# Kernel optimization log

Hardware: AMD Instinct MI355X
Metric: run time of the kernel (lower is better)

Reference implementation:

```python
import jax, jax.numpy as jnp
import numpy as np

TEMPERATURE = 0.5
EPS = 1e-8  # torch CosineSimilarity eps


def setup_inputs() -> dict:
    key = jax.random.key(0)
    k1, k2 = jax.random.split(key)
    N, D = 4096, 256
    z1 = jax.random.normal(k1, (N, D), dtype=jnp.float32)
    z2 = jax.random.normal(k2, (N, D), dtype=jnp.float32)
    return {"z1": z1, "z2": z2}


def reference(z1, z2):
    N = z1.shape[0]
    z = jnp.concatenate([z1, z2], axis=0)  # [2N, D]
    # cosine similarity = normalized dot products (GEMM instead of O(N^2 D) broadcast)
    norm = jnp.linalg.norm(z, axis=-1, keepdims=True)
    zn = z / jnp.maximum(norm, EPS)
    sim = (zn @ zn.T) / TEMPERATURE  # [2N, 2N]
    # mask self-similarity on the diagonal
    idx = jnp.arange(2 * N)
    sim = jnp.where(idx[:, None] == idx[None, :], -jnp.inf, sim)
    # target[i] = (i - N) mod 2N  (arange(2N).roll(N))
    target = jnp.roll(idx, N)
    logp = jax.nn.log_softmax(sim, axis=-1)
    loss = -jnp.mean(logp[idx, target])
    return loss
```

## Files before the change

kernel.cpp:

```cpp
#include <hip/hip_runtime.h>

typedef __bf16 bf16x8 __attribute__((ext_vector_type(8)));
typedef float f32x4 __attribute__((ext_vector_type(4)));

#define TWO_LOG2E 2.88539008177792681f

#define GLOADLDS16(g, l) __builtin_amdgcn_global_load_lds(                     \
    (const __attribute__((address_space(1))) void*)(g),                        \
    (__attribute__((address_space(3))) void*)(l), 16, 0, 0)

__device__ __forceinline__ unsigned f2bf(float f) {
    unsigned u = __float_as_uint(f);
    return (u + 0x7FFFu + ((u >> 16) & 1u)) >> 16;
}

__global__ void __launch_bounds__(256) normalize_kernel(
    const float* __restrict__ z1, const float* __restrict__ z2,
    unsigned short* __restrict__ zn, float* __restrict__ S, float* __restrict__ out)
{
    if (blockIdx.x < 32) S[(blockIdx.x << 8) + threadIdx.x] = 0.f;
    if (blockIdx.x == 32 && threadIdx.x == 0) out[0] = 0.f;

    const int wave = threadIdx.x >> 6, lane = threadIdx.x & 63;
    const int row = (blockIdx.x << 2) + wave;
    const float* src = (row < 4096) ? (z1 + row * 256) : (z2 + (row - 4096) * 256);
    float4 v = ((const float4*)src)[lane];
    float ss = v.x * v.x + v.y * v.y + v.z * v.z + v.w * v.w;
#pragma unroll
    for (int m = 32; m > 0; m >>= 1) ss += __shfl_xor(ss, m, 64);
    float sc = 1.0f / fmaxf(sqrtf(ss), 1e-8f);
    uint2 w;
    w.x = f2bf(v.x * sc) | (f2bf(v.y * sc) << 16);
    w.y = f2bf(v.z * sc) | (f2bf(v.w * sc) << 16);
    *(uint2*)(zn + row * 256 + (lane << 2)) = w;
}

__global__ void __launch_bounds__(64, 2) simexp_kernel(
    const unsigned short* __restrict__ zn, float* __restrict__ S)
{
    __shared__ __align__(16) unsigned short Bs[4][1024];

    const int lane = threadIdx.x;
    const int q = lane >> 4, n16 = lane & 15;
    const int job = blockIdx.x;
    const int rowBase = (job >> 4) << 6;
    const int colRun  = (job & 15) << 9;

    bf16x8 a[4][8];
#pragma unroll
    for (int rt = 0; rt < 4; ++rt)
#pragma unroll
        for (int ks = 0; ks < 8; ++ks)
            a[rt][ks] = *(const bf16x8*)(zn + ((rowBase + (rt << 4) + n16) << 8)
                                            + (ks << 5) + (q << 3));

    auto stage = [&](int m) {
        const int colBase = colRun + ((m >> 3) << 5);
        const int koff = (m & 7) << 5;
        unsigned short* base = (unsigned short*)&Bs[0][0] + ((m & 3) << 10);
#pragma unroll
        for (int p = 0; p < 2; ++p) {
            int s = (p << 6) + lane;
            int c = s >> 2, d = s & 3;
            int k8 = d ^ (c & 3);
            GLOADLDS16(zn + ((colBase + c) << 8) + koff + (k8 << 3), base + (s << 3));
        }
    };

    float rs[4][4];
#pragma unroll
    for (int i = 0; i < 4; ++i)
#pragma unroll
        for (int j = 0; j < 4; ++j) rs[i][j] = 0.f;

    f32x4 acc[4][2];
    auto consume = [&](int m) {
        const unsigned short* bb = (const unsigned short*)&Bs[0][0] + ((m & 3) << 10);
        const int kc = m & 7;
        bf16x8 bf[2];
#pragma unroll
        for (int ct = 0; ct < 2; ++ct) {
            int c = (ct << 4) + n16;
            int d = q ^ (c & 3);
            bf[ct] = *(const bf16x8*)(bb + (((c << 2) | d) << 3));
        }
#pragma unroll
        for (int rt = 0; rt < 4; ++rt)
#pragma unroll
            for (int ct = 0; ct < 2; ++ct)
                acc[rt][ct] = __builtin_amdgcn_mfma_f32_16x16x32_bf16(
                    a[rt][kc], bf[ct], acc[rt][ct], 0, 0, 0);
    };
    auto acczero = [&]() {
#pragma unroll
        for (int rt = 0; rt < 4; ++rt)
#pragma unroll
            for (int ct = 0; ct < 2; ++ct) acc[rt][ct] = (f32x4){0.f, 0.f, 0.f, 0.f};
    };
    auto epilogue = [&]() {
#pragma unroll
        for (int rt = 0; rt < 4; ++rt)
#pragma unroll
            for (int ct = 0; ct < 2; ++ct)
#pragma unroll
                for (int r = 0; r < 4; ++r)
                    rs[rt][r] += __builtin_amdgcn_exp2f(acc[rt][ct][r] * TWO_LOG2E);
    };

    stage(0); stage(1); stage(2);

    for (int cc = 0; cc < 15; ++cc) {
        acczero();
#pragma unroll
        for (int kc = 0; kc < 8; ++kc) {
            int m = (cc << 3) + kc;
            stage(m + 3);
            asm volatile("s_waitcnt vmcnt(6)" ::: "memory");
            consume(m);
        }
        epilogue();
    }
    acczero();
#pragma unroll
    for (int kc = 0; kc < 5; ++kc) {
        int m = 120 + kc;
        stage(m + 3);
        asm volatile("s_waitcnt vmcnt(6)" ::: "memory");
        consume(m);
    }
    asm volatile("s_waitcnt vmcnt(4)" ::: "memory");
    consume(125);
    asm volatile("s_waitcnt vmcnt(2)" ::: "memory");
    consume(126);
    asm volatile("s_waitcnt vmcnt(0)" ::: "memory");
    consume(127);
    epilogue();

#pragma unroll
    for (int rt = 0; rt < 4; ++rt)
#pragma unroll
        for (int r = 0; r < 4; ++r) {
            float s = rs[rt][r];
            s += __shfl_xor(s, 1, 64);
            s += __shfl_xor(s, 2, 64);
            s += __shfl_xor(s, 4, 64);
            s += __shfl_xor(s, 8, 64);
            if (n16 == 0) atomicAdd(&S[rowBase + (rt << 4) + (q << 2) + r], s);
        }
}

__global__ void __launch_bounds__(256) finish_kernel(
    const unsigned short* __restrict__ zn, const float* __restrict__ S,
    float* __restrict__ out)
{
    __shared__ float vals[16];
    const int tid = threadIdx.x, lane = tid & 63, wave = tid >> 6;
    const int q = lane >> 4, n16 = lane & 15;
    const int rib = (wave << 2) + q;
    const int row = (blockIdx.x << 4) + rib;
    const int tar = (row + 4096) & 8191;

    float drr = 0.f, drt = 0.f;
#pragma unroll
    for (int i = 0; i < 4; ++i) {
        int k = (i << 6) + (n16 << 2);
        uint2 ur = *(const uint2*)(zn + (row << 8) + k);
        uint2 ut = *(const uint2*)(zn + (tar << 8) + k);
        float a0 = __uint_as_float(ur.x << 16),  a1 = __uint_as_float(ur.x & 0xFFFF0000u);
        float a2 = __uint_as_float(ur.y << 16),  a3 = __uint_as_float(ur.y & 0xFFFF0000u);
        float b0 = __uint_as_float(ut.x << 16),  b1 = __uint_as_float(ut.x & 0xFFFF0000u);
        float b2 = __uint_as_float(ut.y << 16),  b3 = __uint_as_float(ut.y & 0xFFFF0000u);
        drr += a0 * a0 + a1 * a1 + a2 * a2 + a3 * a3;
        drt += a0 * b0 + a1 * b1 + a2 * b2 + a3 * b3;
    }
#pragma unroll
    for (int m = 1; m <= 8; m <<= 1) {
        drr += __shfl_xor(drr, m, 64);
        drt += __shfl_xor(drt, m, 64);
    }
    if (n16 == 0) {
        float Sv = S[row] - __builtin_amdgcn_exp2f(drr * TWO_LOG2E);
        vals[rib] = 0.693147180559945f * __builtin_amdgcn_logf(Sv) - 2.0f * drt;
    }
    __syncthreads();
    if (tid == 0) {
        float s = 0.f;
#pragma unroll
        for (int i = 0; i < 16; ++i) s += vals[i];
        atomicAdd(out, s * (1.0f / 8192.0f));
    }
}

extern "C" void kernel_launch(void* const* d_in, const int* in_sizes, int n_in,
                              void* d_out, int out_size, void* d_ws, size_t ws_size,
                              hipStream_t stream)
{
    const float* z1 = (const float*)d_in[0];
    const float* z2 = (const float*)d_in[1];
    unsigned short* zn = (unsigned short*)d_ws;
    float* S = (float*)((char*)d_ws + 8192 * 256 * sizeof(unsigned short));
    float* out = (float*)d_out;

    normalize_kernel<<<2048, 256, 0, stream>>>(z1, z2, zn, S, out);
    simexp_kernel<<<2048, 64, 0, stream>>>(zn, S);
    finish_kernel<<<512, 256, 0, stream>>>(zn, S, out);
}
```

Measured before the change: 106.8 us.

## Fuse normalize, sim-exp and finish into one cooperative kernel with grid syncs

Merges the three kernels into a single cooperative launch of 512 blocks of 256 threads, with each wave running one former simexp job and grid-wide syncs between the normalize, GEMM-exp and finish phases. This removes two kernel launch boundaries and their gaps. In exchange, parallelism drops from 2048 single-wave blocks to 512 four-wave blocks that must all be co-resident, and grid syncs add barrier cost. Host-side device queries also add per-call overhead, and the old three-kernel path stays as a fallback.

Measured after the change: 105.8 us. About the same (-0.9%).

```diff
diff --git a/kernel.cpp b/kernel.cpp
--- a/kernel.cpp
+++ b/kernel.cpp
@@ -1,4 +1,7 @@
 #include <hip/hip_runtime.h>
+#include <hip/hip_cooperative_groups.h>
+
+namespace cg = cooperative_groups;
 
 typedef __bf16 bf16x8 __attribute__((ext_vector_type(8)));
 typedef float f32x4 __attribute__((ext_vector_type(4)));
@@ -14,35 +17,12 @@
     return (u + 0x7FFFu + ((u >> 16) & 1u)) >> 16;
 }
 
-__global__ void __launch_bounds__(256) normalize_kernel(
-    const float* __restrict__ z1, const float* __restrict__ z2,
-    unsigned short* __restrict__ zn, float* __restrict__ S, float* __restrict__ out)
-{
-    if (blockIdx.x < 32) S[(blockIdx.x << 8) + threadIdx.x] = 0.f;
-    if (blockIdx.x == 32 && threadIdx.x == 0) out[0] = 0.f;
-
-    const int wave = threadIdx.x >> 6, lane = threadIdx.x & 63;
-    const int row = (blockIdx.x << 2) + wave;
-    const float* src = (row < 4096) ? (z1 + row * 256) : (z2 + (row - 4096) * 256);
-    float4 v = ((const float4*)src)[lane];
-    float ss = v.x * v.x + v.y * v.y + v.z * v.z + v.w * v.w;
-#pragma unroll
-    for (int m = 32; m > 0; m >>= 1) ss += __shfl_xor(ss, m, 64);
-    float sc = 1.0f / fmaxf(sqrtf(ss), 1e-8f);
-    uint2 w;
-    w.x = f2bf(v.x * sc) | (f2bf(v.y * sc) << 16);
-    w.y = f2bf(v.z * sc) | (f2bf(v.w * sc) << 16);
-    *(uint2*)(zn + row * 256 + (lane << 2)) = w;
-}
-
-__global__ void __launch_bounds__(64, 2) simexp_kernel(
-    const unsigned short* __restrict__ zn, float* __restrict__ S)
-{
-    __shared__ __align__(16) unsigned short Bs[4][1024];
-
-    const int lane = threadIdx.x;
+__device__ __forceinline__ void simexp_wave(const unsigned short* __restrict__ zn,
+                                            float* __restrict__ S,
+                                            unsigned short* __restrict__ ring,
+                                            int job, int lane)
+{
     const int q = lane >> 4, n16 = lane & 15;
-    const int job = blockIdx.x;
     const int rowBase = (job >> 4) << 6;
     const int colRun  = (job & 15) << 9;
 
@@ -57,7 +37,7 @@
     auto stage = [&](int m) {
         const int colBase = colRun + ((m >> 3) << 5);
         const int koff = (m & 7) << 5;
-        unsigned short* base = (unsigned short*)&Bs[0][0] + ((m & 3) << 10);
+        unsigned short* base = ring + ((m & 3) << 10);
 #pragma unroll
         for (int p = 0; p < 2; ++p) {
             int s = (p << 6) + lane;
@@ -75,7 +55,7 @@
 
     f32x4 acc[4][2];
     auto consume = [&](int m) {
-        const unsigned short* bb = (const unsigned short*)&Bs[0][0] + ((m & 3) << 10);
+        const unsigned short* bb = ring + ((m & 3) << 10);
         const int kc = m & 7;
         bf16x8 bf[2];
 #pragma unroll
@@ -149,17 +129,43 @@
         }
 }
 
-__global__ void __launch_bounds__(256) finish_kernel(
-    const unsigned short* __restrict__ zn, const float* __restrict__ S,
-    float* __restrict__ out)
-{
-    __shared__ float vals[16];
+__global__ void __launch_bounds__(256, 2) ntxent_fused(
+    const float* __restrict__ z1, const float* __restrict__ z2,
+    unsigned short* __restrict__ zn, float* __restrict__ S, float* __restrict__ out)
+{
+    __shared__ __align__(16) unsigned short Bs[4][4][1024];
+
     const int tid = threadIdx.x, lane = tid & 63, wave = tid >> 6;
     const int q = lane >> 4, n16 = lane & 15;
+    const int b = blockIdx.x;
+
+    if (tid < 16) S[(b << 4) + tid] = 0.f;
+    if (b == 0 && tid == 0) out[0] = 0.f;
+#pragma unroll
+    for (int r = 0; r < 4; ++r) {
+        int row = (b << 4) + (wave << 2) + r;
+        const float* src = (row < 4096) ? (z1 + row * 256) : (z2 + (row - 4096) * 256);
+        float4 v = ((const float4*)src)[lane];
+        float ss = v.x * v.x + v.y * v.y + v.z * v.z + v.w * v.w;
+#pragma unroll
+        for (int m = 32; m > 0; m >>= 1) ss += __shfl_xor(ss, m, 64);
+        float sc = 1.0f / fmaxf(sqrtf(ss), 1e-8f);
+        uint2 w;
+        w.x = f2bf(v.x * sc) | (f2bf(v.y * sc) << 16);
+        w.y = f2bf(v.z * sc) | (f2bf(v.w * sc) << 16);
+        *(uint2*)(zn + row * 256 + (lane << 2)) = w;
+    }
+
+    cg::this_grid().sync();
+
+    simexp_wave(zn, S, &Bs[wave][0][0], (b << 2) | wave, lane);
+
+    cg::this_grid().sync();
+
+    float* vals = (float*)&Bs[0][0][0];
     const int rib = (wave << 2) + q;
-    const int row = (blockIdx.x << 4) + rib;
+    const int row = (b << 4) + rib;
     const int tar = (row + 4096) & 8191;
-
     float drr = 0.f, drt = 0.f;
 #pragma unroll
     for (int i = 0; i < 4; ++i) {
@@ -178,6 +184,75 @@
         drr += __shfl_xor(drr, m, 64);
         drt += __shfl_xor(drt, m, 64);
     }
+    __syncthreads();
+    if (n16 == 0) {
+        float Sv = S[row] - __builtin_amdgcn_exp2f(drr * TWO_LOG2E);
+        vals[rib] = 0.693147180559945f * __builtin_amdgcn_logf(Sv) - 2.0f * drt;
+    }
+    __syncthreads();
+    if (tid == 0) {
+        float s = 0.f;
+#pragma unroll
+        for (int i = 0; i < 16; ++i) s += vals[i];
+        atomicAdd(out, s * (1.0f / 8192.0f));
+    }
+}
+
+__global__ void __launch_bounds__(256) normalize_kernel(
+    const float* __restrict__ z1, const float* __restrict__ z2,
+    unsigned short* __restrict__ zn, float* __restrict__ S, float* __restrict__ out)
+{
+    if (blockIdx.x < 32) S[(blockIdx.x << 8) + threadIdx.x] = 0.f;
+    if (blockIdx.x == 32 && threadIdx.x == 0) out[0] = 0.f;
+    const int wave = threadIdx.x >> 6, lane = threadIdx.x & 63;
+    const int row = (blockIdx.x << 2) + wave;
+    const float* src = (row < 4096) ? (z1 + row * 256) : (z2 + (row - 4096) * 256);
+    float4 v = ((const float4*)src)[lane];
+    float ss = v.x * v.x + v.y * v.y + v.z * v.z + v.w * v.w;
+#pragma unroll
+    for (int m = 32; m > 0; m >>= 1) ss += __shfl_xor(ss, m, 64);
+    float sc = 1.0f / fmaxf(sqrtf(ss), 1e-8f);
+    uint2 w;
+    w.x = f2bf(v.x * sc) | (f2bf(v.y * sc) << 16);
+    w.y = f2bf(v.z * sc) | (f2bf(v.w * sc) << 16);
+    *(uint2*)(zn + row * 256 + (lane << 2)) = w;
+}
+
+__global__ void __launch_bounds__(64, 2) simexp_kernel(
+    const unsigned short* __restrict__ zn, float* __restrict__ S)
+{
+    __shared__ __align__(16) unsigned short Bs[4][1024];
+    simexp_wave(zn, S, &Bs[0][0], blockIdx.x, threadIdx.x);
+}
+
+__global__ void __launch_bounds__(256) finish_kernel(
+    const unsigned short* __restrict__ zn, const float* __restrict__ S,
+    float* __restrict__ out)
+{
+    __shared__ float vals[16];
+    const int tid = threadIdx.x, lane = tid & 63, wave = tid >> 6;
+    const int q = lane >> 4, n16 = lane & 15;
+    const int rib = (wave << 2) + q;
+    const int row = (blockIdx.x << 4) + rib;
+    const int tar = (row + 4096) & 8191;
+    float drr = 0.f, drt = 0.f;
+#pragma unroll
+    for (int i = 0; i < 4; ++i) {
+        int k = (i << 6) + (n16 << 2);
+        uint2 ur = *(const uint2*)(zn + (row << 8) + k);
+        uint2 ut = *(const uint2*)(zn + (tar << 8) + k);
+        float a0 = __uint_as_float(ur.x << 16),  a1 = __uint_as_float(ur.x & 0xFFFF0000u);
+        float a2 = __uint_as_float(ur.y << 16),  a3 = __uint_as_float(ur.y & 0xFFFF0000u);
+        float b0 = __uint_as_float(ut.x << 16),  b1 = __uint_as_float(ut.x & 0xFFFF0000u);
+        float b2 = __uint_as_float(ut.y << 16),  b3 = __uint_as_float(ut.y & 0xFFFF0000u);
+        drr += a0 * a0 + a1 * a1 + a2 * a2 + a3 * a3;
+        drt += a0 * b0 + a1 * b1 + a2 * b2 + a3 * b3;
+    }
+#pragma unroll
+    for (int m = 1; m <= 8; m <<= 1) {
+        drr += __shfl_xor(drr, m, 64);
+        drt += __shfl_xor(drt, m, 64);
+    }
     if (n16 == 0) {
         float Sv = S[row] - __builtin_amdgcn_exp2f(drr * TWO_LOG2E);
         vals[rib] = 0.693147180559945f * __builtin_amdgcn_logf(Sv) - 2.0f * drt;
@@ -201,6 +276,21 @@
     float* S = (float*)((char*)d_ws + 8192 * 256 * sizeof(unsigned short));
     float* out = (float*)d_out;
 
+    int dev = 0;
+    hipGetDevice(&dev);
+    int coopOK = 0;
+    hipDeviceGetAttribute(&coopOK, hipDeviceAttributeCooperativeLaunch, dev);
+    int cus = 0;
+    hipDeviceGetAttribute(&cus, hipDeviceAttributeMultiprocessorCount, dev);
+    int maxB = 0;
+    hipOccupancyMaxActiveBlocksPerMultiprocessor(&maxB, ntxent_fused, 256, 0);
+
+    if (coopOK && (long long)maxB * cus >= 512) {
+        void* args[] = {(void*)&z1, (void*)&z2, (void*)&zn, (void*)&S, (void*)&out};
+        hipError_t err = hipLaunchCooperativeKernel(ntxent_fused, dim3(512), dim3(256),
+                                                    args, 0, stream);
+        if (err == hipSuccess) return;
+    }
     normalize_kernel<<<2048, 256, 0, stream>>>(z1, z2, zn, S, out);
     simexp_kernel<<<2048, 64, 0, stream>>>(zn, S);
     finish_kernel<<<512, 256, 0, stream>>>(zn, S, out);
```

## Exploit symmetry of similarity matrix to compute only upper-triangular tiles

Applied to the files above, without the earlier changes.

The exp-sum kernel now computes only the upper-triangular blocks of the symmetric similarity matrix. Each tile's exponentials are added both to its row sums and, via column sums reduced across lanes, to the sums of the transposed rows. Diagonal-straddling tiles mask entries by index so nothing is counted twice. This roughly halves the MFMA and exp work in exchange for extra column-sum atomics, a per-element index compare on diagonal tiles, and a 2112-block grid of half-length column runs.

After: 144.6 us. +35.3%, slower.

```diff
diff --git a/kernel.cpp b/kernel.cpp
--- a/kernel.cpp
+++ b/kernel.cpp
@@ -42,9 +42,14 @@
 
     const int lane = threadIdx.x;
     const int q = lane >> 4, n16 = lane & 15;
-    const int job = blockIdx.x;
-    const int rowBase = (job >> 4) << 6;
-    const int colRun  = (job & 15) << 9;
+
+    int t = blockIdx.x, v = 0;
+    while (t >= ((32 - v) << 2)) { t -= (32 - v) << 2; ++v; }
+    const int si = (v << 2) + t / (32 - v);
+    const int rn = v + t % (32 - v);
+    const int rowBase = si << 6;
+    const int colRun  = rn << 8;
+    const bool strad = (rn == v);
 
     bf16x8 a[4][8];
 #pragma unroll
@@ -68,10 +73,13 @@
     };
 
     float rs[4][4];
+    float cs[16];
 #pragma unroll
     for (int i = 0; i < 4; ++i)
 #pragma unroll
         for (int j = 0; j < 4; ++j) rs[i][j] = 0.f;
+#pragma unroll
+    for (int i = 0; i < 16; ++i) cs[i] = 0.f;
 
     f32x4 acc[4][2];
     auto consume = [&](int m) {
@@ -97,19 +105,38 @@
 #pragma unroll
             for (int ct = 0; ct < 2; ++ct) acc[rt][ct] = (f32x4){0.f, 0.f, 0.f, 0.f};
     };
-    auto epilogue = [&]() {
-#pragma unroll
-        for (int rt = 0; rt < 4; ++rt)
-#pragma unroll
-            for (int ct = 0; ct < 2; ++ct)
-#pragma unroll
-                for (int r = 0; r < 4; ++r)
-                    rs[rt][r] += __builtin_amdgcn_exp2f(acc[rt][ct][r] * TWO_LOG2E);
+    auto epilogue = [&](int cc) {
+        if (!strad) {
+#pragma unroll
+            for (int rt = 0; rt < 4; ++rt)
+#pragma unroll
+                for (int ct = 0; ct < 2; ++ct)
+#pragma unroll
+                    for (int r = 0; r < 4; ++r) {
+                        float e = __builtin_amdgcn_exp2f(acc[rt][ct][r] * TWO_LOG2E);
+                        rs[rt][r] += e;
+                        cs[(cc << 1) + ct] += e;
+                    }
+        } else {
+#pragma unroll
+            for (int rt = 0; rt < 4; ++rt)
+#pragma unroll
+                for (int ct = 0; ct < 2; ++ct) {
+                    int j = colRun + (cc << 5) + (ct << 4) + n16;
+#pragma unroll
+                    for (int r = 0; r < 4; ++r) {
+                        float e = __builtin_amdgcn_exp2f(acc[rt][ct][r] * TWO_LOG2E);
+                        int i = rowBase + (rt << 4) + (q << 2) + r;
+                        rs[rt][r] += (j >= i) ? e : 0.f;
+                        cs[(cc << 1) + ct] += (j > i) ? e : 0.f;
+                    }
+                }
+        }
     };
 
     stage(0); stage(1); stage(2);
 
-    for (int cc = 0; cc < 15; ++cc) {
+    for (int cc = 0; cc < 7; ++cc) {
         acczero();
 #pragma unroll
         for (int kc = 0; kc < 8; ++kc) {
@@ -118,23 +145,23 @@
             asm volatile("s_waitcnt vmcnt(6)" ::: "memory");
             consume(m);
         }
-        epilogue();
+        epilogue(cc);
     }
     acczero();
 #pragma unroll
     for (int kc = 0; kc < 5; ++kc) {
-        int m = 120 + kc;
+        int m = 56 + kc;
         stage(m + 3);
         asm volatile("s_waitcnt vmcnt(6)" ::: "memory");
         consume(m);
     }
     asm volatile("s_waitcnt vmcnt(4)" ::: "memory");
-    consume(125);
+    consume(61);
     asm volatile("s_waitcnt vmcnt(2)" ::: "memory");
-    consume(126);
+    consume(62);
     asm volatile("s_waitcnt vmcnt(0)" ::: "memory");
-    consume(127);
-    epilogue();
+    consume(63);
+    epilogue(7);
 
 #pragma unroll
     for (int rt = 0; rt < 4; ++rt)
@@ -147,6 +174,14 @@
             s += __shfl_xor(s, 8, 64);
             if (n16 == 0) atomicAdd(&S[rowBase + (rt << 4) + (q << 2) + r], s);
         }
+#pragma unroll
+    for (int idx = 0; idx < 16; ++idx) {
+        float s = cs[idx];
+        s += __shfl_xor(s, 16, 64);
+        s += __shfl_xor(s, 32, 64);
+        if (q == 0)
+            atomicAdd(&S[colRun + ((idx >> 1) << 5) + ((idx & 1) << 4) + n16], s);
+    }
 }
 
 __global__ void __launch_bounds__(256) finish_kernel(
@@ -202,6 +237,6 @@
     float* out = (float*)d_out;
 
     normalize_kernel<<<2048, 256, 0, stream>>>(z1, z2, zn, S, out);
-    simexp_kernel<<<2048, 64, 0, stream>>>(zn, S);
+    simexp_kernel<<<2112, 64, 0, stream>>>(zn, S);
     finish_kernel<<<512, 256, 0, stream>>>(zn, S, out);
 }
```
